# Kernel optimization log

Measured on AMD Instinct MI355X. Metric: run time of the kernel, lower is better.

Reference implementation:

```python
import jax, jax.numpy as jnp
import numpy as np

IOU_THR = 0.5
TOP_K = 10
D_MODEL = 256
BS, NQ = 8, 1000


def _layer_norm(x, g, b, eps=1e-5):
    m = x.mean(-1, keepdims=True)
    v = ((x - m) ** 2).mean(-1, keepdims=True)
    return (x - m) * jax.lax.rsqrt(v + eps) * g + b


def _box_iou(boxes):
    # boxes: [nq, 4] xyxy; pairwise IoU [nq, nq]
    area = (boxes[:, 2] - boxes[:, 0]) * (boxes[:, 3] - boxes[:, 1])
    lt = jnp.maximum(boxes[:, None, :2], boxes[None, :, :2])
    rb = jnp.minimum(boxes[:, None, 2:], boxes[None, :, 2:])
    wh = jnp.clip(rb - lt, 0.0)
    inter = wh[..., 0] * wh[..., 1]
    union = area[:, None] + area[None, :] - inter
    return inter / union


def setup_inputs() -> dict:
    key = jax.random.key(0)
    ks = jax.random.split(key, 16)
    d = D_MODEL
    s = 1.0 / np.sqrt(d)
    tgt = jax.random.normal(ks[0], (BS, NQ, d), dtype=jnp.float32)
    seed_mask = (jax.random.uniform(ks[1], (BS, NQ, 1)) < 0.2).astype(jnp.float32)
    # cxcywh boxes in (0,1) with positive wh
    cxy = jax.random.uniform(ks[2], (BS, NQ, 2), minval=0.1, maxval=0.9)
    wh = jax.random.uniform(ks[3], (BS, NQ, 2), minval=0.05, maxval=0.3)
    pred_boxes = jnp.concatenate([cxy, wh], axis=-1).astype(jnp.float32)
    def lin(k):
        kw, kb = jax.random.split(k)
        return (jax.random.uniform(kw, (d, d), minval=-s, maxval=s, dtype=jnp.float32),
                jax.random.uniform(kb, (d,), minval=-s, maxval=s, dtype=jnp.float32))
    W1, b1 = lin(ks[4]); W2, b2 = lin(ks[5]); W3, b3 = lin(ks[6])
    W4, b4 = lin(ks[7]); W5, b5 = lin(ks[8])
    g2 = jnp.ones((d,), jnp.float32); be2 = jnp.zeros((d,), jnp.float32)
    return {"tgt": tgt, "seed_mask": seed_mask, "pred_boxes": pred_boxes,
            "W1": W1, "b1": b1, "W2": W2, "b2": b2, "g2": g2, "be2": be2,
            "W3": W3, "b3": b3, "W4": W4, "b4": b4, "W5": W5, "b5": b5}


def reference(tgt, seed_mask, pred_boxes, W1, b1, W2, b2, g2, be2, W3, b3, W4, b4, W5, b5):
    bs, nq, d = tgt.shape
    # cxcywh -> xyxy
    cxy, wh = pred_boxes[..., :2], pred_boxes[..., 2:]
    box_xyxy = jnp.concatenate([cxy - 0.5 * wh, cxy + 0.5 * wh], axis=-1)
    ious = jax.vmap(_box_iou)(box_xyxy)                       # [bs,nq,nq]
    attn_mask = ious >= IOU_THR
    neg_mask = 1.0 - seed_mask                                # [bs,nq,1]
    # mask out non-seed columns and seed rows
    overlaps = ious * jnp.swapaxes(seed_mask, 1, 2) * neg_mask  # [bs,nq,nq]
    idx = jnp.argsort(-overlaps, axis=-1)[..., :TOP_K]        # [bs,nq,k]
    nmk = jnp.take_along_axis(
        jnp.broadcast_to(jnp.swapaxes(seed_mask, 1, 2), (bs, nq, nq)), idx, axis=2)
    ious_g = jnp.take_along_axis(overlaps, idx, axis=2)       # [bs,nq,k]
    mk = nmk * (ious_g >= IOU_THR).astype(tgt.dtype)          # [bs,nq,k]
    # id token MLP + layernorm
    id_token = _layer_norm(jax.nn.relu(tgt @ W1 + b1) @ W2 + b2, g2, be2)
    # neighbor gather: [bs,nq,k,d]
    neighbors_id = jax.vmap(lambda t, i: t[i])(id_token, idx)
    id_feature = id_token[:, :, None, :] - neighbors_id
    features = jax.nn.relu(id_feature @ W3 + b3) @ W4 + b4
    cur_tgt = (features * mk[..., None]).max(axis=2)          # [bs,nq,d]
    cur_tgt = tgt + jax.nn.relu(cur_tgt @ W5 + b5) * neg_mask
    return cur_tgt, attn_mask
```

## Files before the change

### kernel.cpp

```cpp
#include <hip/hip_runtime.h>
#include <hip/hip_bf16.h>

#define BSZ   8
#define NQ    1000
#define DM    256
#define MROWS (BSZ*NQ)
#define TOPK  10
#define NTILE (MROWS/16)

typedef __attribute__((ext_vector_type(8))) short short8;
typedef __attribute__((ext_vector_type(4))) float f32x4;
typedef unsigned short u16;
typedef unsigned int   u32;

static __device__ __forceinline__ float b2f(u16 u) { return __uint_as_float(((u32)u) << 16); }
static __device__ __forceinline__ u16 f2b(float f) {
    __hip_bfloat16 h = __float2bfloat16(f);
    return *(u16*)&h;
}
static __device__ __forceinline__ u32 encf(float f) {
    u32 u = __float_as_uint(f);
    return (u & 0x80000000u) ? ~u : (u | 0x80000000u);
}
static __device__ __forceinline__ float decf(u32 e) {
    u32 u = (e & 0x80000000u) ? (e ^ 0x80000000u) : ~e;
    return __uint_as_float(u);
}

__global__ __launch_bounds__(256) void prep_k(
    const float* __restrict__ W1, const float* __restrict__ W2,
    const float* __restrict__ W3, const float* __restrict__ W4,
    const float* __restrict__ W5, u16* __restrict__ WT)
{
    const int m  = blockIdx.x >> 4;
    const int kb = (blockIdx.x & 15) * 16;
    const float* W = (m==0)?W1:(m==1)?W2:(m==2)?W3:(m==3)?W4:W5;
    u16* D = WT + (size_t)m * DM * DM;
    const int t = threadIdx.x;
    u16 tmp[16];
    #pragma unroll
    for (int kk = 0; kk < 16; ++kk)
        tmp[kk] = f2b(W[(size_t)(kb+kk)*DM + t]);
    #pragma unroll
    for (int kk = 0; kk < 16; ++kk)
        D[(size_t)t*DM + kb + kk] = tmp[kk];
}

template<int EPI>
static __device__ __forceinline__ void block_gemm256(
    const u16 (*__restrict__ A)[264], const u16* __restrict__ WT,
    const float* __restrict__ bias, u16 (*__restrict__ OutL)[264],
    u16* __restrict__ OutG, float* __restrict__ OutF,
    const float* __restrict__ tgt, const float* __restrict__ seed,
    int r0, u16 (*__restrict__ W_lds)[72], int t)
{
    const int lane = t & 63, wave = t >> 6;
    const int m = lane & 15, quad = lane >> 4;
    f32x4 acc[4];
    #pragma unroll
    for (int nt = 0; nt < 4; ++nt)
        #pragma unroll
        for (int i = 0; i < 4; ++i) acc[nt][i] = 0.f;
    for (int kc = 0; kc < 4; ++kc) {
        __syncthreads();
        #pragma unroll
        for (int pass = 0; pass < 8; ++pass) {
            const int n = pass*32 + (t >> 3), ko = (t & 7) * 8;
            *(uint4*)&W_lds[n][ko] = *(const uint4*)&WT[(size_t)n*DM + kc*64 + ko];
        }
        __syncthreads();
        #pragma unroll
        for (int ks = 0; ks < 2; ++ks) {
            const short8 a = *(const short8*)&A[m][kc*64 + ks*32 + quad*8];
            #pragma unroll
            for (int nt = 0; nt < 4; ++nt) {
                const int n = wave*64 + nt*16 + m;
                const short8 b = *(const short8*)&W_lds[n][ks*32 + quad*8];
                acc[nt] = __builtin_amdgcn_mfma_f32_16x16x32_bf16(a, b, acc[nt], 0, 0, 0);
            }
        }
    }
    #pragma unroll
    for (int nt = 0; nt < 4; ++nt) {
        const int n = wave*64 + nt*16 + m;
        const float bb = bias ? bias[n] : 0.f;
        #pragma unroll
        for (int reg = 0; reg < 4; ++reg) {
            const int rl = quad*4 + reg;
            float v = acc[nt][reg] + bb;
            if (EPI == 0) OutL[rl][n] = f2b(fmaxf(v, 0.f));
            if (EPI == 1) OutL[rl][n] = f2b(v);
            if (EPI == 2) OutG[(size_t)(r0+rl)*DM + n] = f2b(v);
            if (EPI == 3) {
                const int R = r0 + rl;
                OutF[(size_t)R*DM + n] = tgt[(size_t)R*DM + n]
                                       + fmaxf(v, 0.f) * (1.f - seed[R]);
            }
        }
    }
}

struct MlpSmem { u16 bufA[16][264]; u16 bufB[16][264]; u16 W_lds[256][72]; };
struct IouSmem { float sv[NQ]; int sj[NQ]; int scount; };

__global__ __launch_bounds__(256) void fused_iou_mlp_k(
    const float* __restrict__ boxes, const float* __restrict__ seed,
    const u16* __restrict__ WT,
    const float* __restrict__ b1, const float* __restrict__ b2,
    const float* __restrict__ g2, const float* __restrict__ be2,
    const float* __restrict__ tgt,
    u16* __restrict__ P, float* __restrict__ attn,
    int* __restrict__ cnt, int* __restrict__ inc0, int* __restrict__ idxs)
{
    __shared__ __align__(16) unsigned char smraw[sizeof(MlpSmem)];
    const int t = threadIdx.x;
    const int bid = blockIdx.x;

    if (bid < NTILE) {
        MlpSmem& sm = *reinterpret_cast<MlpSmem*>(smraw);
        const int r0 = bid * 16;
        const int lane = t & 63, wave = t >> 6;
        const u16* W1T = WT;
        const u16* W2T = WT + (size_t)1*DM*DM;
        const u16* W3T = WT + (size_t)2*DM*DM;

        {
            const int r = t >> 4, c0 = (t & 15) * 16;
            const float* src = &tgt[(size_t)(r0 + r)*DM + c0];
            __align__(16) u16 h[16];
            #pragma unroll
            for (int q = 0; q < 4; ++q) {
                const float4 f = *(const float4*)&src[q*4];
                h[q*4+0] = f2b(f.x); h[q*4+1] = f2b(f.y);
                h[q*4+2] = f2b(f.z); h[q*4+3] = f2b(f.w);
            }
            *(uint4*)&sm.bufA[r][c0]     = *(uint4*)&h[0];
            *(uint4*)&sm.bufA[r][c0 + 8] = *(uint4*)&h[8];
        }

        block_gemm256<0>(sm.bufA, W1T, b1, sm.bufB,
                         nullptr, nullptr, nullptr, nullptr, r0, sm.W_lds, t);
        block_gemm256<1>(sm.bufB, W2T, b2, sm.bufA,
                         nullptr, nullptr, nullptr, nullptr, r0, sm.W_lds, t);
        __syncthreads();
        for (int rr = 0; rr < 4; ++rr) {
            const int row = wave*4 + rr;
            float x[4];
            #pragma unroll
            for (int i = 0; i < 4; ++i) x[i] = b2f(sm.bufA[row][lane + 64*i]);
            float s = x[0]+x[1]+x[2]+x[3];
            float q = x[0]*x[0]+x[1]*x[1]+x[2]*x[2]+x[3]*x[3];
            #pragma unroll
            for (int off = 32; off; off >>= 1) {
                s += __shfl_down(s, off, 64);
                q += __shfl_down(q, off, 64);
            }
            s = __shfl(s, 0, 64); q = __shfl(q, 0, 64);
            const float mn  = s * (1.f/DM);
            const float vr  = q * (1.f/DM) - mn*mn;
            const float inv = rsqrtf(vr + 1e-5f);
            #pragma unroll
            for (int i = 0; i < 4; ++i) {
                const int c = lane + 64*i;
                sm.bufA[row][c] = f2b((x[i]-mn)*inv*g2[c] + be2[c]);
            }
        }
        block_gemm256<2>(sm.bufA, W3T, nullptr, nullptr,
                         P, nullptr, nullptr, nullptr, r0, sm.W_lds, t);
        return;
    }

    {
        #pragma clang fp contract(off)
        IouSmem& sm = *reinterpret_cast<IouSmem*>(smraw);
        const int row = bid - NTILE;
        const int b   = row / NQ;
        if (t == 0) sm.scount = 0;

        const float* bi = boxes + (size_t)row * 4;
        const float icx = bi[0], icy = bi[1], iw = bi[2], ih = bi[3];
        const float ix0 = icx - 0.5f*iw, iy0 = icy - 0.5f*ih;
        const float ix1 = icx + 0.5f*iw, iy1 = icy + 0.5f*ih;
        const float area_i = (ix1-ix0)*(iy1-iy0);
        const float neg_i  = 1.f - seed[row];
        __syncthreads();

        float* arow = attn + (size_t)row * NQ;
        for (int j = t; j < NQ; j += 256) {
            const float* bj = boxes + (size_t)(b*NQ + j) * 4;
            const float cx = bj[0], cy = bj[1], w = bj[2], h = bj[3];
            const float x0 = cx - 0.5f*w, y0 = cy - 0.5f*h;
            const float x1 = cx + 0.5f*w, y1 = cy + 0.5f*h;
            const float area_j = (x1-x0)*(y1-y0);
            const float ltx = fmaxf(ix0, x0), lty = fmaxf(iy0, y0);
            const float rbx = fminf(ix1, x1), rby = fminf(iy1, y1);
            const float wx = fmaxf(rbx-ltx, 0.f), wy = fmaxf(rby-lty, 0.f);
            const float inter = wx*wy;
            const float uni = (area_i + area_j) - inter;
            const float iou = inter / uni;
            arow[j] = (iou >= 0.5f) ? 1.0f : 0.0f;
            const float ov = (iou * seed[b*NQ + j]) * neg_i;
            if (ov >= 0.5f) {
                const int p = atomicAdd(&sm.scount, 1);
                if (p < NQ) { sm.sv[p] = ov; sm.sj[p] = j; }
            }
        }
        __syncthreads();

        if (t == 0) {
            const int n = sm.scount;
            inc0[row] = (n < TOPK) ? 1 : 0;
            if (n <= TOPK) {
                cnt[row] = n;
                for (int k = 0; k < n; ++k) idxs[row*TOPK + k] = b*NQ + sm.sj[k];
            } else {
                float bv[TOPK]; int bj[TOPK];
                #pragma unroll
                for (int k = 0; k < TOPK; ++k) { bv[k] = -1.f; bj[k] = 0x7fffffff; }
                for (int e = 0; e < n; ++e) {
                    const float v = sm.sv[e]; const int j = sm.sj[e];
                    int w = 0;
                    #pragma unroll
                    for (int k = 1; k < TOPK; ++k)
                        if (bv[k] < bv[w] || (bv[k] == bv[w] && bj[k] > bj[w])) w = k;
                    if (v > bv[w] || (v == bv[w] && j < bj[w])) { bv[w] = v; bj[w] = j; }
                }
                cnt[row] = TOPK;
                for (int k = 0; k < TOPK; ++k) idxs[row*TOPK + k] = b*NQ + bj[k];
            }
        }
    }
}

__global__ __launch_bounds__(256) void pairs_final_k(
    const u16* __restrict__ P, const u16* __restrict__ WT,
    const float* __restrict__ b3, const float* __restrict__ b4,
    const float* __restrict__ b5,
    const int* __restrict__ cnt, const int* __restrict__ inc0,
    const int* __restrict__ idxs,
    const float* __restrict__ tgt, const float* __restrict__ seed,
    float* __restrict__ out)
{
    __shared__ __align__(16) u16 U[16][264];
    __shared__ __align__(16) u16 W_lds[256][72];
    __shared__ u32 cmU[16][264];
    __shared__ int pl_rl[176], pl_j[176];
    __shared__ int sInc[16];
    __shared__ int np;
    const int t = threadIdx.x, r0 = blockIdx.x * 16;
    const int lane = t & 63, wave = t >> 6;
    const int m = lane & 15, quad = lane >> 4;
    const u16* W4T = WT + (size_t)3*DM*DM;
    const u16* W5T = WT + (size_t)4*DM*DM;

    if (t == 0) np = 0;
    __syncthreads();
    if (t < 16) {
        const int r = r0 + t;
        int c = cnt[r];
        c = (c < 0) ? 0 : ((c > TOPK) ? TOPK : c);
        sInc[t] = inc0[r];
        const int base = atomicAdd(&np, c);
        for (int k = 0; k < c; ++k) {
            pl_rl[base + k] = t;
            int j = idxs[r*TOPK + k];
            j = (j < 0) ? 0 : ((j >= MROWS) ? MROWS-1 : j);
            pl_j[base + k] = j;
        }
    }
    __syncthreads();
    const int npairs = np;
    #pragma unroll
    for (int rl2 = 0; rl2 < 16; ++rl2)
        cmU[rl2][t] = sInc[rl2] ? 0x80000000u  : encf(-3.402823466e38f);
    const float bb3 = b3[t];

    for (int pc = 0; pc*16 < npairs; ++pc) {
        #pragma unroll
        for (int pp = 0; pp < 16; ++pp) {
            const int pr = pc*16 + pp;
            u16 uv = 0;
            if (pr < npairs) {
                const int i = r0 + pl_rl[pr];
                const int j = pl_j[pr];
                uv = f2b(fmaxf(b2f(P[(size_t)i*DM + t]) - b2f(P[(size_t)j*DM + t]) + bb3, 0.f));
            }
            U[pp][t] = uv;
        }
        f32x4 acc[4];
        #pragma unroll
        for (int nt = 0; nt < 4; ++nt)
            #pragma unroll
            for (int i = 0; i < 4; ++i) acc[nt][i] = 0.f;
        for (int kc = 0; kc < 4; ++kc) {
            __syncthreads();
            #pragma unroll
            for (int pass = 0; pass < 8; ++pass) {
                const int n = pass*32 + (t >> 3), ko = (t & 7) * 8;
                *(uint4*)&W_lds[n][ko] = *(const uint4*)&W4T[(size_t)n*DM + kc*64 + ko];
            }
            __syncthreads();
            #pragma unroll
            for (int ks = 0; ks < 2; ++ks) {
                const short8 a = *(const short8*)&U[m][kc*64 + ks*32 + quad*8];
                #pragma unroll
                for (int nt = 0; nt < 4; ++nt) {
                    const int n = wave*64 + nt*16 + m;
                    const short8 b = *(const short8*)&W_lds[n][ks*32 + quad*8];
                    acc[nt] = __builtin_amdgcn_mfma_f32_16x16x32_bf16(a, b, acc[nt], 0, 0, 0);
                }
            }
        }
        #pragma unroll
        for (int nt = 0; nt < 4; ++nt) {
            const int n = wave*64 + nt*16 + m;
            const float bb4 = b4[n];
            #pragma unroll
            for (int reg = 0; reg < 4; ++reg) {
                const int pr = pc*16 + quad*4 + reg;
                if (pr < npairs) {
                    const int rl2 = pl_rl[pr];
                    atomicMax(&cmU[rl2][n], encf(acc[nt][reg] + bb4));
                }
            }
        }
    }
    __syncthreads();
    #pragma unroll
    for (int rl2 = 0; rl2 < 16; ++rl2)
        U[rl2][t] = f2b(decf(cmU[rl2][t]));
    block_gemm256<3>(U, W5T, b5, nullptr, nullptr, out,
                     tgt, seed, r0, W_lds, t);
}

extern "C" void kernel_launch(void* const* d_in, const int* in_sizes, int n_in,
                              void* d_out, int out_size, void* d_ws, size_t ws_size,
                              hipStream_t stream)
{
    (void)in_sizes; (void)n_in; (void)out_size; (void)ws_size;
    const float* tgt   = (const float*)d_in[0];
    const float* seed  = (const float*)d_in[1];
    const float* boxes = (const float*)d_in[2];
    const float* W1 = (const float*)d_in[3];
    const float* b1 = (const float*)d_in[4];
    const float* W2 = (const float*)d_in[5];
    const float* b2 = (const float*)d_in[6];
    const float* g2 = (const float*)d_in[7];
    const float* be2= (const float*)d_in[8];
    const float* W3 = (const float*)d_in[9];
    const float* b3 = (const float*)d_in[10];
    const float* W4 = (const float*)d_in[11];
    const float* b4 = (const float*)d_in[12];
    const float* W5 = (const float*)d_in[13];
    const float* b5 = (const float*)d_in[14];

    float* out_tgt  = (float*)d_out;
    float* out_attn = out_tgt + (size_t)MROWS * DM;

    u16* WT   = (u16*)d_ws;
    u16* P    = WT + (size_t)5*DM*DM;
    int* cnt  = (int*)(P + (size_t)MROWS*DM);
    int* inc0 = cnt + MROWS;
    int* idxs = inc0 + MROWS;

    prep_k<<<80, 256, 0, stream>>>(W1, W2, W3, W4, W5, WT);
    fused_iou_mlp_k<<<NTILE + MROWS, 256, 0, stream>>>(
        boxes, seed, WT, b1, b2, g2, be2, tgt, P, out_attn, cnt, inc0, idxs);
    pairs_final_k<<<MROWS/16, 256, 0, stream>>>(P, WT, b3, b4, b5, cnt, inc0, idxs,
                                                tgt, seed, out_tgt);
}
```

Baseline: 149.3 us.

## Load GEMM weight fragments directly from global memory instead of staging through LDS

```diff
diff --git a/kernel.cpp b/kernel.cpp
--- a/kernel.cpp
+++ b/kernel.cpp
@@ -52,7 +52,7 @@
     const float* __restrict__ bias, u16 (*__restrict__ OutL)[264],
     u16* __restrict__ OutG, float* __restrict__ OutF,
     const float* __restrict__ tgt, const float* __restrict__ seed,
-    int r0, u16 (*__restrict__ W_lds)[72], int t)
+    int r0, int t)
 {
     const int lane = t & 63, wave = t >> 6;
     const int m = lane & 15, quad = lane >> 4;
@@ -61,21 +61,15 @@
     for (int nt = 0; nt < 4; ++nt)
         #pragma unroll
         for (int i = 0; i < 4; ++i) acc[nt][i] = 0.f;
+    __syncthreads();
+    const u16* Wb = WT + (size_t)(wave*64 + m)*DM + quad*8;
     for (int kc = 0; kc < 4; ++kc) {
-        __syncthreads();
-        #pragma unroll
-        for (int pass = 0; pass < 8; ++pass) {
-            const int n = pass*32 + (t >> 3), ko = (t & 7) * 8;
-            *(uint4*)&W_lds[n][ko] = *(const uint4*)&WT[(size_t)n*DM + kc*64 + ko];
-        }
-        __syncthreads();
         #pragma unroll
         for (int ks = 0; ks < 2; ++ks) {
             const short8 a = *(const short8*)&A[m][kc*64 + ks*32 + quad*8];
             #pragma unroll
             for (int nt = 0; nt < 4; ++nt) {
-                const int n = wave*64 + nt*16 + m;
-                const short8 b = *(const short8*)&W_lds[n][ks*32 + quad*8];
+                const short8 b = *(const short8*)&Wb[(size_t)nt*16*DM + kc*64 + ks*32];
                 acc[nt] = __builtin_amdgcn_mfma_f32_16x16x32_bf16(a, b, acc[nt], 0, 0, 0);
             }
         }
@@ -100,10 +94,10 @@
     }
 }
 
-struct MlpSmem { u16 bufA[16][264]; u16 bufB[16][264]; u16 W_lds[256][72]; };
+struct MlpSmem { u16 bufA[16][264]; u16 bufB[16][264]; };
 struct IouSmem { float sv[NQ]; int sj[NQ]; int scount; };
 
-__global__ __launch_bounds__(256) void fused_iou_mlp_k(
+__global__ __launch_bounds__(256, 4) void fused_iou_mlp_k(
     const float* __restrict__ boxes, const float* __restrict__ seed,
     const u16* __restrict__ WT,
     const float* __restrict__ b1, const float* __restrict__ b2,
@@ -139,9 +133,9 @@
         }
 
         block_gemm256<0>(sm.bufA, W1T, b1, sm.bufB,
-                         nullptr, nullptr, nullptr, nullptr, r0, sm.W_lds, t);
+                         nullptr, nullptr, nullptr, nullptr, r0, t);
         block_gemm256<1>(sm.bufB, W2T, b2, sm.bufA,
-                         nullptr, nullptr, nullptr, nullptr, r0, sm.W_lds, t);
+                         nullptr, nullptr, nullptr, nullptr, r0, t);
         __syncthreads();
         for (int rr = 0; rr < 4; ++rr) {
             const int row = wave*4 + rr;
@@ -166,7 +160,7 @@
             }
         }
         block_gemm256<2>(sm.bufA, W3T, nullptr, nullptr,
-                         P, nullptr, nullptr, nullptr, r0, sm.W_lds, t);
+                         P, nullptr, nullptr, nullptr, r0, t);
         return;
     }
 
@@ -232,7 +226,7 @@
     }
 }
 
-__global__ __launch_bounds__(256) void pairs_final_k(
+__global__ __launch_bounds__(256, 4) void pairs_final_k(
     const u16* __restrict__ P, const u16* __restrict__ WT,
     const float* __restrict__ b3, const float* __restrict__ b4,
     const float* __restrict__ b5,
@@ -242,7 +236,6 @@
     float* __restrict__ out)
 {
     __shared__ __align__(16) u16 U[16][264];
-    __shared__ __align__(16) u16 W_lds[256][72];
     __shared__ u32 cmU[16][264];
     __shared__ int pl_rl[176], pl_j[176];
     __shared__ int sInc[16];
@@ -274,6 +267,7 @@
     for (int rl2 = 0; rl2 < 16; ++rl2)
         cmU[rl2][t] = sInc[rl2] ? 0x80000000u  : encf(-3.402823466e38f);
     const float bb3 = b3[t];
+    const u16* W4b = W4T + (size_t)(wave*64 + m)*DM + quad*8;
 
     for (int pc = 0; pc*16 < npairs; ++pc) {
         #pragma unroll
@@ -287,26 +281,19 @@
             }
             U[pp][t] = uv;
         }
+        __syncthreads();
         f32x4 acc[4];
         #pragma unroll
         for (int nt = 0; nt < 4; ++nt)
             #pragma unroll
             for (int i = 0; i < 4; ++i) acc[nt][i] = 0.f;
         for (int kc = 0; kc < 4; ++kc) {
-            __syncthreads();
-            #pragma unroll
-            for (int pass = 0; pass < 8; ++pass) {
-                const int n = pass*32 + (t >> 3), ko = (t & 7) * 8;
-                *(uint4*)&W_lds[n][ko] = *(const uint4*)&W4T[(size_t)n*DM + kc*64 + ko];
-            }
-            __syncthreads();
             #pragma unroll
             for (int ks = 0; ks < 2; ++ks) {
                 const short8 a = *(const short8*)&U[m][kc*64 + ks*32 + quad*8];
                 #pragma unroll
                 for (int nt = 0; nt < 4; ++nt) {
-                    const int n = wave*64 + nt*16 + m;
-                    const short8 b = *(const short8*)&W_lds[n][ks*32 + quad*8];
+                    const short8 b = *(const short8*)&W4b[(size_t)nt*16*DM + kc*64 + ks*32];
                     acc[nt] = __builtin_amdgcn_mfma_f32_16x16x32_bf16(a, b, acc[nt], 0, 0, 0);
                 }
             }
@@ -324,13 +311,14 @@
                 }
             }
         }
+        __syncthreads();
     }
     __syncthreads();
     #pragma unroll
     for (int rl2 = 0; rl2 < 16; ++rl2)
         U[rl2][t] = f2b(decf(cmU[rl2][t]));
     block_gemm256<3>(U, W5T, b5, nullptr, nullptr, out,
-                     tgt, seed, r0, W_lds, t);
+                     tgt, seed, r0, t);
 }
 
 extern "C" void kernel_launch(void* const* d_in, const int* in_sizes, int n_in,
```

Measured after the change: 165.0 us. +10.5%, slower.
